# Kernel tuning notes

Hardware: AMD Instinct MI355X
Metric: run time of the kernel (lower is better)

Reference implementation:

```python
import jax, jax.numpy as jnp
import numpy as np

EPS = 1e-8  # torch F.cosine_similarity clamps norms at eps=1e-8


def setup_inputs() -> dict:
    key = jax.random.key(0)
    N, M, D = 1024, 20, 768  # speakers, utterances/speaker, embed dim
    embeddings = jax.random.normal(key, (N, M, D), dtype=jnp.float32)
    w = jnp.asarray(10.0, dtype=jnp.float32)  # init_w
    b = jnp.asarray(-5.0, dtype=jnp.float32)  # init_b
    return {"embeddings": embeddings, "w": w, "b": b}


def reference(embeddings, w, b):
    N, M, D = embeddings.shape
    centroids = embeddings.mean(axis=1)  # [N, D]
    # cosine similarity as one fused GEMM on normalized vectors
    e = embeddings / jnp.maximum(
        jnp.linalg.norm(embeddings, axis=-1, keepdims=True), EPS)
    c = centroids / jnp.maximum(
        jnp.linalg.norm(centroids, axis=-1, keepdims=True), EPS)
    # sim[j, i, m] = cos(e[i, m], centroid[j])  -- matches the torch loop/stack
    sim = jnp.einsum('imd,jd->jim', e, c)
    logits = w * sim + b  # [N_j, N_i, M]
    # torch: view(N*N, M).transpose(0,1).reshape(-1, N)
    #   => row index r = m*N + j, column i
    logits = jnp.transpose(logits, (2, 0, 1)).reshape(N * M, N)
    # torch labels: arange(N) expanded over M -> labels[r] = r // M
    labels = jnp.repeat(jnp.arange(N), M)
    logp = jax.nn.log_softmax(logits, axis=-1)
    loss = -jnp.mean(logp[jnp.arange(N * M), labels])
    return loss
```

## Files before the change

### kernel.cpp

```cpp
#include <hip/hip_runtime.h>
#include <hip/hip_bf16.h>
#include <cstdint>

#define N_SPK 1024
#define M_UTT 20
#define D_DIM 768
#define NM_ROWS (N_SPK * M_UTT)

static constexpr float EPS = 1e-8f;

#define WAIT_VM0   0x0F70
#define WAIT_VM16  0x4F70
#define WAIT_LGKM0 0xC07F

typedef __attribute__((ext_vector_type(4))) float floatx4;

__device__ __forceinline__ void load16_to_lds(const void* g, void* l) {
    __builtin_amdgcn_global_load_lds(
        (const __attribute__((address_space(1))) uint32_t*)g,
        (__attribute__((address_space(3))) uint32_t*)l, 16, 0, 0);
}

__device__ __forceinline__ float wave_sum(float v) {
    #pragma unroll
    for (int o = 32; o > 0; o >>= 1) v += __shfl_xor(v, o);
    return v;
}

__device__ __forceinline__ unsigned short fp8pk(float a, float b) {
    return (unsigned short)(__builtin_amdgcn_cvt_pk_fp8_f32(a, b, 0, false) & 0xFFFF);
}

__global__ __launch_bounds__(384) void prep_kernel(const float* __restrict__ emb,
                                                   unsigned char* __restrict__ ehat,
                                                   unsigned char* __restrict__ chat,
                                                   int* __restrict__ ctr,
                                                   float* __restrict__ accum) {
    const int i = blockIdx.x;
    const int t = threadIdx.x;
    const int wave = t >> 6, lane = t & 63;

    if (i == 0 && t == 0) { *ctr = 0; *accum = 0.f; }

    const float2* src = (const float2*)(emb + (size_t)i * M_UTT * D_DIM);

    float2 v[M_UTT];
    float ss[M_UTT];
    float2 cen = {0.f, 0.f};
    #pragma unroll
    for (int m = 0; m < M_UTT; ++m) {
        const float2 x = src[m * 384 + t];
        v[m] = x;
        ss[m] = x.x * x.x + x.y * x.y;
        cen.x += x.x; cen.y += x.y;
    }
    cen.x *= (1.f / M_UTT); cen.y *= (1.f / M_UTT);
    float css = cen.x * cen.x + cen.y * cen.y;

    __shared__ float red[M_UTT + 1][6];
    #pragma unroll
    for (int m = 0; m < M_UTT; ++m) {
        const float s = wave_sum(ss[m]);
        if (lane == 0) red[m][wave] = s;
    }
    {
        const float s = wave_sum(css);
        if (lane == 0) red[M_UTT][wave] = s;
    }
    __syncthreads();

    #pragma unroll
    for (int m = 0; m < M_UTT; ++m) {
        const float tot = red[m][0] + red[m][1] + red[m][2] +
                          red[m][3] + red[m][4] + red[m][5];
        const float rn = 1.0f / fmaxf(sqrtf(tot), EPS);
        ((unsigned short*)(ehat + ((size_t)(m * N_SPK + i)) * D_DIM))[t] =
            fp8pk(v[m].x * rn, v[m].y * rn);
    }
    {
        const float tot = red[M_UTT][0] + red[M_UTT][1] + red[M_UTT][2] +
                          red[M_UTT][3] + red[M_UTT][4] + red[M_UTT][5];
        const float rn = 1.0f / fmaxf(sqrtf(tot), EPS);
        ((unsigned short*)(chat + (size_t)i * D_DIM))[t] =
            fp8pk(cen.x * rn, cen.y * rn);
    }
}

__global__ __launch_bounds__(64) void gemm_fused_kernel(
        const unsigned char* __restrict__ ehat,
        const unsigned char* __restrict__ chat,
        const float* __restrict__ wp,
        float* __restrict__ Psum,
        float* __restrict__ T) {
    __shared__ unsigned char As[2][64 * 128];
    __shared__ unsigned char Bs[2][64 * 128];

    const int lane = threadIdx.x;
    const int c = lane & 15;
    const int quad = lane >> 4;

    const int xcd = blockIdx.x & 7;
    const int idx = blockIdx.x >> 3;
    const int bu  = xcd * 40 + (idx >> 4);
    const int bj  = idx & 15;
    const int m   = bu >> 4;
    const int rb  = bu & 15;
    const int u0  = bu * 64;
    const int j0  = bj * 64;

    const unsigned char* Ag = ehat + (size_t)u0 * D_DIM;
    const unsigned char* Bg = chat + (size_t)j0 * D_DIM;

    int goff[8];
    #pragma unroll
    for (int s = 0; s < 8; ++s) {
        const int ci  = s * 64 + lane;
        const int row = ci >> 3;
        const int q   = (ci & 7) ^ (row & 7);
        goff[s] = row * D_DIM + q * 16;
    }

    int slotA[4][4], slotB[4][4];
    #pragma unroll
    for (int ks = 0; ks < 4; ++ks) {
        const int q = ks * 2 + (quad >> 1);
        #pragma unroll
        for (int f = 0; f < 4; ++f) {
            const int r = f * 16 + c;
            slotA[ks][f] = (r * 8 + (q ^ (r & 7))) * 16 + (quad & 1) * 8;
            slotB[ks][f] = slotA[ks][f];
        }
    }

    floatx4 acc[4][4] = {};

    #pragma unroll
    for (int s = 0; s < 8; ++s) {
        load16_to_lds(Ag + goff[s],       As[0] + (s * 64 + lane) * 16);
        load16_to_lds(Bg + goff[s],       Bs[0] + (s * 64 + lane) * 16);
    }
    #pragma unroll
    for (int s = 0; s < 8; ++s) {
        load16_to_lds(Ag + goff[s] + 128, As[1] + (s * 64 + lane) * 16);
        load16_to_lds(Bg + goff[s] + 128, Bs[1] + (s * 64 + lane) * 16);
    }

    #pragma unroll
    for (int kt = 0; kt < 6; ++kt) {
        if (kt < 5) __builtin_amdgcn_s_waitcnt(WAIT_VM16);
        else        __builtin_amdgcn_s_waitcnt(WAIT_VM0);

        const unsigned char* Ab = As[kt & 1];
        const unsigned char* Bb = Bs[kt & 1];

        #pragma unroll
        for (int ks = 0; ks < 4; ++ks) {
            long af[4], bf[4];
            #pragma unroll
            for (int it = 0; it < 4; ++it)
                af[it] = *(const long*)(Ab + slotA[ks][it]);
            #pragma unroll
            for (int jt = 0; jt < 4; ++jt)
                bf[jt] = *(const long*)(Bb + slotB[ks][jt]);

            #pragma unroll
            for (int it = 0; it < 4; ++it)
                #pragma unroll
                for (int jt = 0; jt < 4; ++jt)
                    acc[it][jt] = __builtin_amdgcn_mfma_f32_16x16x32_fp8_fp8(
                        af[it], bf[jt], acc[it][jt], 0, 0, 0);
        }

        if (kt < 4) {
            const int k0 = (kt + 2) * 128;
            __builtin_amdgcn_s_waitcnt(WAIT_LGKM0);
            #pragma unroll
            for (int s = 0; s < 8; ++s) {
                load16_to_lds(Ag + goff[s] + k0, As[kt & 1] + (s * 64 + lane) * 16);
                load16_to_lds(Bg + goff[s] + k0, Bs[kt & 1] + (s * 64 + lane) * 16);
            }
        }
    }

    const float w = wp[0];

    #pragma unroll
    for (int jt = 0; jt < 4; ++jt) {
        float sm = 0.f;
        #pragma unroll
        for (int it = 0; it < 4; ++it)
            #pragma unroll
            for (int r = 0; r < 4; ++r)
                sm += __expf(w * (acc[it][jt][r] - 1.0f));
        sm += __shfl_xor(sm, 16);
        sm += __shfl_xor(sm, 32);
        if (quad == 0) Psum[(size_t)bu * N_SPK + j0 + jt * 16 + c] = sm;
    }

    #pragma unroll
    for (int it = 0; it < 4; ++it) {
        #pragma unroll
        for (int jt = 0; jt < 4; ++jt) {
            const int col = j0 + jt * 16 + c;
            const int g = m * N_SPK + col;
            const int istar = g / M_UTT;
            const int rloc = rb * 64 + it * 16 + quad * 4;
            #pragma unroll
            for (int r = 0; r < 4; ++r) {
                if (rloc + r == istar) T[g] = acc[it][jt][r];
            }
        }
    }
}

__global__ void combine_kernel(const float* __restrict__ Psum,
                               const float* __restrict__ T,
                               const float* __restrict__ wp,
                               int* __restrict__ ctr,
                               float* __restrict__ accum,
                               float* __restrict__ out) {
    const int p = blockIdx.x * 256 + threadIdx.x;
    const int m = p >> 10;
    const int j = p & 1023;
    const float w = wp[0];

    float S = 0.f;
    #pragma unroll
    for (int rb = 0; rb < 16; ++rb)
        S += Psum[(size_t)(m * 16 + rb) * N_SPK + j];
    const float term = w * (T[p] - 1.0f) - __logf(S);

    __shared__ float red[256];
    red[threadIdx.x] = term;
    __syncthreads();
    for (int o = 128; o > 0; o >>= 1) {
        if (threadIdx.x < o) red[threadIdx.x] += red[threadIdx.x + o];
        __syncthreads();
    }
    if (threadIdx.x == 0) {
        atomicAdd(accum, red[0]);
        __threadfence();
        const int old = atomicAdd(ctr, 1);
        if (old == 79) {
            const float a = atomicAdd(accum, 0.0f);
            out[0] = -a / (float)NM_ROWS;
        }
    }
}

extern "C" void kernel_launch(void* const* d_in, const int* in_sizes, int n_in,
                              void* d_out, int out_size, void* d_ws, size_t ws_size,
                              hipStream_t stream) {
    const float* emb = (const float*)d_in[0];
    const float* wp  = (const float*)d_in[1];
    float* out = (float*)d_out;

    char* ws = (char*)d_ws;
    unsigned char* ehat = (unsigned char*)(ws);
    unsigned char* chat = (unsigned char*)(ws + 15728640);
    float* Psum  = (float*)(ws + 16515072);
    float* T     = (float*)(ws + 17825792);
    int*   ctr   = (int*)  (ws + 17907712);
    float* accum = (float*)(ws + 17907716);

    prep_kernel<<<dim3(N_SPK), dim3(384), 0, stream>>>(emb, ehat, chat, ctr, accum);
    gemm_fused_kernel<<<dim3(5120), dim3(64), 0, stream>>>(ehat, chat, wp, Psum, T);
    combine_kernel<<<dim3(80), dim3(256), 0, stream>>>(Psum, T, wp, ctr, accum, out);
}
```

Before: 154.2 us.

## Load centroid GEMM operand directly into registers instead of staging through LDS

The B operand (normalized centroids) is now fetched from global memory straight into a double-buffered register array instead of being copied into LDS and read back, which halves LDS traffic and footprint. The vmcnt wait threshold is raised so it accounts for the extra in-flight register loads, and the MFMA block gets a higher wave priority via s_setprio plus sched barriers. The cost is many more VGPRs held for breg and 8-byte global loads that are not coalesced, which may lower occupancy or add latency.

```diff
diff --git a/kernel.cpp b/kernel.cpp
--- a/kernel.cpp
+++ b/kernel.cpp
@@ -10,7 +10,7 @@
 static constexpr float EPS = 1e-8f;
 
 #define WAIT_VM0   0x0F70
-#define WAIT_VM16  0x4F70
+#define WAIT_VM24  0x4F78
 #define WAIT_LGKM0 0xC07F
 
 typedef __attribute__((ext_vector_type(4))) float floatx4;
@@ -93,7 +93,6 @@
         float* __restrict__ Psum,
         float* __restrict__ T) {
     __shared__ unsigned char As[2][64 * 128];
-    __shared__ unsigned char Bs[2][64 * 128];
 
     const int lane = threadIdx.x;
     const int c = lane & 15;
@@ -120,7 +119,7 @@
         goff[s] = row * D_DIM + q * 16;
     }
 
-    int slotA[4][4], slotB[4][4];
+    int slotA[4][4];
     #pragma unroll
     for (int ks = 0; ks < 4; ++ks) {
         const int q = ks * 2 + (quad >> 1);
@@ -128,57 +127,75 @@
         for (int f = 0; f < 4; ++f) {
             const int r = f * 16 + c;
             slotA[ks][f] = (r * 8 + (q ^ (r & 7))) * 16 + (quad & 1) * 8;
-            slotB[ks][f] = slotA[ks][f];
-        }
-    }
+        }
+    }
+
+    int boff[4][4];
+    #pragma unroll
+    for (int ks = 0; ks < 4; ++ks)
+        #pragma unroll
+        for (int jt = 0; jt < 4; ++jt)
+            boff[ks][jt] = (jt * 16 + c) * D_DIM
+                         + (ks * 2 + (quad >> 1)) * 16 + (quad & 1) * 8;
 
     floatx4 acc[4][4] = {};
-
-    #pragma unroll
-    for (int s = 0; s < 8; ++s) {
-        load16_to_lds(Ag + goff[s],       As[0] + (s * 64 + lane) * 16);
-        load16_to_lds(Bg + goff[s],       Bs[0] + (s * 64 + lane) * 16);
-    }
-    #pragma unroll
-    for (int s = 0; s < 8; ++s) {
+    long breg[2][4][4];
+
+    #pragma unroll
+    for (int s = 0; s < 8; ++s)
+        load16_to_lds(Ag + goff[s], As[0] + (s * 64 + lane) * 16);
+    #pragma unroll
+    for (int ks = 0; ks < 4; ++ks)
+        #pragma unroll
+        for (int jt = 0; jt < 4; ++jt)
+            breg[0][ks][jt] = *(const long*)(Bg + boff[ks][jt]);
+    #pragma unroll
+    for (int s = 0; s < 8; ++s)
         load16_to_lds(Ag + goff[s] + 128, As[1] + (s * 64 + lane) * 16);
-        load16_to_lds(Bg + goff[s] + 128, Bs[1] + (s * 64 + lane) * 16);
-    }
+    #pragma unroll
+    for (int ks = 0; ks < 4; ++ks)
+        #pragma unroll
+        for (int jt = 0; jt < 4; ++jt)
+            breg[1][ks][jt] = *(const long*)(Bg + boff[ks][jt] + 128);
+    __builtin_amdgcn_sched_barrier(0);
 
     #pragma unroll
     for (int kt = 0; kt < 6; ++kt) {
-        if (kt < 5) __builtin_amdgcn_s_waitcnt(WAIT_VM16);
-        else        __builtin_amdgcn_s_waitcnt(WAIT_VM0);
+        if (kt <= 4) __builtin_amdgcn_s_waitcnt(WAIT_VM24);
+        else         __builtin_amdgcn_s_waitcnt(WAIT_VM0);
+        __builtin_amdgcn_sched_barrier(0);
 
         const unsigned char* Ab = As[kt & 1];
-        const unsigned char* Bb = Bs[kt & 1];
-
+
+        __builtin_amdgcn_s_setprio(1);
         #pragma unroll
         for (int ks = 0; ks < 4; ++ks) {
-            long af[4], bf[4];
+            long af[4];
             #pragma unroll
             for (int it = 0; it < 4; ++it)
                 af[it] = *(const long*)(Ab + slotA[ks][it]);
-            #pragma unroll
-            for (int jt = 0; jt < 4; ++jt)
-                bf[jt] = *(const long*)(Bb + slotB[ks][jt]);
 
             #pragma unroll
             for (int it = 0; it < 4; ++it)
                 #pragma unroll
                 for (int jt = 0; jt < 4; ++jt)
                     acc[it][jt] = __builtin_amdgcn_mfma_f32_16x16x32_fp8_fp8(
-                        af[it], bf[jt], acc[it][jt], 0, 0, 0);
-        }
+                        af[it], breg[kt & 1][ks][jt], acc[it][jt], 0, 0, 0);
+        }
+        __builtin_amdgcn_s_setprio(0);
 
         if (kt < 4) {
             const int k0 = (kt + 2) * 128;
             __builtin_amdgcn_s_waitcnt(WAIT_LGKM0);
             #pragma unroll
-            for (int s = 0; s < 8; ++s) {
+            for (int s = 0; s < 8; ++s)
                 load16_to_lds(Ag + goff[s] + k0, As[kt & 1] + (s * 64 + lane) * 16);
-                load16_to_lds(Bg + goff[s] + k0, Bs[kt & 1] + (s * 64 + lane) * 16);
-            }
+            #pragma unroll
+            for (int ks = 0; ks < 4; ++ks)
+                #pragma unroll
+                for (int jt = 0; jt < 4; ++jt)
+                    breg[kt & 1][ks][jt] = *(const long*)(Bg + boff[ks][jt] + k0);
+            __builtin_amdgcn_sched_barrier(0);
         }
     }
 
```

After: 170.7 us. +10.7%, slower.
